# Kernel tuning notes

Measured on AMD Instinct MI355X. Metric: run time of the kernel, lower is better.

Reference implementation:

```python
import jax, jax.numpy as jnp
import numpy as np

B, T, D = 2, 2048, 2048
H, HD = 32, 64  # n_heads, head_dim; H*HD == attn_dim == D


def _rope(x, cos, sin):
    # x: (B,T,H,HD) with interleaved (real, imag) pairs on last dim
    b, t, h, hd = x.shape
    x2 = x.reshape(b, t, h, hd // 2, 2)
    xr, xi = x2[..., 0], x2[..., 1]
    c = cos[None, :, None, :]  # (1,T,1,HD/2)
    s = sin[None, :, None, :]
    out_r = xr * c - xi * s
    out_i = xr * s + xi * c
    return jnp.stack([out_r, out_i], axis=-1).reshape(b, t, h, hd)


def setup_inputs() -> dict:
    key = jax.random.key(0)
    ks = jax.random.split(key, 5)
    x = jax.random.normal(ks[0], (B, T, D), dtype=jnp.float32)
    scale = 0.02
    wq = jax.random.normal(ks[1], (D, D), dtype=jnp.float32) * scale
    wk = jax.random.normal(ks[2], (D, D), dtype=jnp.float32) * scale
    wv = jax.random.normal(ks[3], (D, D), dtype=jnp.float32) * scale
    wo = jax.random.normal(ks[4], (D, D), dtype=jnp.float32) * scale
    # standard RoPE frequencies, theta = 10000
    inv_freq = 1.0 / (10000.0 ** (jnp.arange(0, HD, 2, dtype=jnp.float32) / HD))  # (HD/2,)
    angles = jnp.arange(T, dtype=jnp.float32)[:, None] * inv_freq[None, :]  # (T, HD/2)
    return {
        "x": x,
        "freqs_cos": jnp.cos(angles),
        "freqs_sin": jnp.sin(angles),
        "wq": wq, "wk": wk, "wv": wv, "wo": wo,
    }


def reference(x, freqs_cos, freqs_sin, wq, wk, wv, wo):
    b, t, d = x.shape
    # fused-style QKV projections (nn.Linear: x @ W.T, no bias)
    q = (x @ wq.T).reshape(b, t, H, HD)
    k = (x @ wk.T).reshape(b, t, H, HD)
    v = (x @ wv.T).reshape(b, t, H, HD)
    q = _rope(q, freqs_cos, freqs_sin)
    k = _rope(k, freqs_cos, freqs_sin)
    # causal SDPA, scale = 1/sqrt(head_dim)
    scale = 1.0 / jnp.sqrt(jnp.float32(HD))
    scores = jnp.einsum("bqhd,bkhd->bhqk", q, k) * scale  # (B,H,T,T)
    causal = jnp.tril(jnp.ones((t, t), dtype=bool))
    scores = jnp.where(causal[None, None], scores, jnp.float32(-jnp.inf))
    attn = jax.nn.softmax(scores, axis=-1)
    y = jnp.einsum("bhqk,bkhd->bqhd", attn, v).reshape(b, t, H * HD)
    return y @ wo.T
```

## Files before the change

### kernel.cpp

```cpp
#include <hip/hip_runtime.h>
#include <hip/hip_bf16.h>
#include <stdint.h>


typedef __bf16 bf16_t;
typedef __bf16 bf16x4 __attribute__((ext_vector_type(4)));
typedef __bf16 bf16x8 __attribute__((ext_vector_type(8)));
typedef float  f32x4  __attribute__((ext_vector_type(4)));

constexpr int B_ = 2, T_ = 2048, D_ = 2048, H_ = 32, HD_ = 64;
constexpr int M_ = B_ * T_;

__device__ __forceinline__ void async_copy16(const bf16_t* g, bf16_t* l) {
  __builtin_amdgcn_global_load_lds(
      (const __attribute__((address_space(1))) void*)g,
      (__attribute__((address_space(3))) void*)l, 16, 0, 0);
}

__global__ __launch_bounds__(256) void cast_f32_bf16(
    const float* __restrict__ src, bf16_t* __restrict__ dst, int n4)
{
  const int i = blockIdx.x * 256 + threadIdx.x;
  if (i >= n4) return;
  const float4 v = ((const float4*)src)[i];
  bf16x4 o;
  o[0] = (bf16_t)v.x; o[1] = (bf16_t)v.y; o[2] = (bf16_t)v.z; o[3] = (bf16_t)v.w;
  ((bf16x4*)dst)[i] = o;
}

template <typename OutT>
__global__ __launch_bounds__(256, 2) void gemm_bt(
    const bf16_t* __restrict__ A, const bf16_t* __restrict__ B,
    OutT* __restrict__ C, int M, int N, int K)
{
  __shared__ __attribute__((aligned(16))) bf16_t As[128 * 32];
  __shared__ __attribute__((aligned(16))) bf16_t Bs[128 * 32];

  const int tid    = threadIdx.x;
  const int w      = tid >> 6;
  const int l      = tid & 63;
  const int quad   = l >> 4;
  const int lane16 = l & 15;
  const int bm0 = blockIdx.x * 128;
  const int bn0 = blockIdx.y * 128;
  const int wm  = (w >> 1) * 64;
  const int wn  = (w & 1) * 64;
  const int srow = l >> 2;
  const int scol = (l & 3) * 8;

  const bf16_t* Ag = A + (size_t)bm0 * K;
  const bf16_t* Bg = B + (size_t)bn0 * K;

  f32x4 acc[4][4] = {};

  for (int kk = 0; kk < K; kk += 32) {
    __syncthreads();
#pragma unroll
    for (int s0 = 0; s0 < 2; ++s0) {
      const int s = w + s0 * 4;
      async_copy16(Ag + (size_t)(s * 16 + srow) * K + kk + scol, &As[s * 512]);
      async_copy16(Bg + (size_t)(s * 16 + srow) * K + kk + scol, &Bs[s * 512]);
    }
    __syncthreads();

    bf16x8 af[4], bfr[4];
#pragma unroll
    for (int i = 0; i < 4; ++i)
      af[i] = *(const bf16x8*)&As[(wm + i * 16 + lane16) * 32 + quad * 8];
#pragma unroll
    for (int j = 0; j < 4; ++j)
      bfr[j] = *(const bf16x8*)&Bs[(wn + j * 16 + lane16) * 32 + quad * 8];
#pragma unroll
    for (int i = 0; i < 4; ++i)
#pragma unroll
      for (int j = 0; j < 4; ++j)
        acc[i][j] = __builtin_amdgcn_mfma_f32_16x16x32_bf16(af[i], bfr[j],
                                                            acc[i][j], 0, 0, 0);
  }

#pragma unroll
  for (int i = 0; i < 4; ++i) {
#pragma unroll
    for (int r = 0; r < 4; ++r) {
      const size_t row = (size_t)(bm0 + wm + i * 16 + quad * 4 + r);
#pragma unroll
      for (int j = 0; j < 4; ++j) {
        const int col = bn0 + wn + j * 16 + lane16;
        C[row * N + col] = (OutT)acc[i][j][r];
      }
    }
  }
}

__global__ __launch_bounds__(256) void rope_kernel(
    bf16_t* __restrict__ q, bf16_t* __restrict__ k,
    const float* __restrict__ cosb, const float* __restrict__ sinb, int npair)
{
  const int idx = blockIdx.x * 256 + threadIdx.x;
  if (idx >= npair) return;
  const int p = idx & 31;
  const int t = (idx >> 10) & (T_ - 1);
  const float c = cosb[t * 32 + p];
  const float s = sinb[t * 32 + p];
  const size_t off = (size_t)idx * 2;

  const float qr = (float)q[off], qi = (float)q[off + 1];
  q[off]     = (bf16_t)((qr * c - qi * s) * 0.125f);
  q[off + 1] = (bf16_t)((qr * s + qi * c) * 0.125f);

  const float kr = (float)k[off], ki = (float)k[off + 1];
  k[off]     = (bf16_t)(kr * c - ki * s);
  k[off + 1] = (bf16_t)(kr * s + ki * c);
}

__global__ __launch_bounds__(256, 3) void flash_attn(
    const bf16_t* __restrict__ Q, const bf16_t* __restrict__ K,
    const bf16_t* __restrict__ V, bf16_t* __restrict__ Y)
{
  __shared__ __attribute__((aligned(16))) bf16_t Kf[4096];
  __shared__ __attribute__((aligned(16))) bf16_t Vf[4096];
  __shared__ __attribute__((aligned(16))) bf16_t Pt[4 * 2 * 16 * 68];

  const int tid    = threadIdx.x;
  const int w      = tid >> 6;
  const int l      = tid & 63;
  const int quad   = l >> 4;
  const int lane16 = l & 15;
  const int bh = blockIdx.y;
  const int b  = bh >> 5;
  const int h  = bh & 31;
  const int q0 = ((int)gridDim.x - 1 - (int)blockIdx.x) * 128;
  const int qa = q0 + w * 32;
  const size_t rs = (size_t)H_ * HD_;

  const bf16_t* Qb = Q + ((size_t)b * T_) * rs + h * HD_;
  const bf16_t* Kb = K + ((size_t)b * T_) * rs + h * HD_;
  const bf16_t* Vb = V + ((size_t)b * T_) * rs + h * HD_;

  bf16x8 qf[2][2];
#pragma unroll
  for (int t = 0; t < 2; ++t)
#pragma unroll
    for (int c = 0; c < 2; ++c)
      qf[t][c] = *(const bf16x8*)(Qb + (size_t)(qa + t * 16 + lane16) * rs +
                                  c * 32 + quad * 8);

  f32x4 o[2][4] = {};
  float lsum[2] = {0.f, 0.f};

  const int koff = tid >> 3;
  const int oct  = tid & 7;
  const int d0   = oct * 8;
  const int kc = oct >> 2, kq = oct & 3;
  const int nV = oct >> 1, base16 = (oct & 1) * 8;

  bf16_t* const PtW = Pt + w * (2 * 16 * 68);

  const int nsteps = q0 / 64 + 2;

  bf16x8 kr[2], vr[2];
#pragma unroll
  for (int hf = 0; hf < 2; ++hf) {
    const int key = hf * 32 + koff;
    kr[hf] = *(const bf16x8*)(Kb + (size_t)key * rs + d0);
    vr[hf] = *(const bf16x8*)(Vb + (size_t)key * rs + d0);
  }

  for (int it = 0; it < nsteps; ++it) {
    const int k0 = it * 64;
    __syncthreads();
#pragma unroll
    for (int hf = 0; hf < 2; ++hf) {
      const int key = hf * 32 + koff;
      const int gK = ((kc * 4 + (key >> 4)) * 16 + (key & 15)) * 4 + kq;
      *(bf16x8*)&Kf[gK * 8] = kr[hf];
      const int cV = key >> 5, qV = (key >> 3) & 3, jV = key & 7;
#pragma unroll
      for (int i = 0; i < 8; ++i) {
        const int g = ((cV * 4 + nV) * 16 + base16 + i) * 4 + qV;
        Vf[(g ^ oct) * 8 + jV] = vr[hf][i];
      }
    }
    __syncthreads();
    if (it + 1 < nsteps) {
      const int k0n = k0 + 64;
#pragma unroll
      for (int hf = 0; hf < 2; ++hf) {
        const int key = k0n + hf * 32 + koff;
        kr[hf] = *(const bf16x8*)(Kb + (size_t)key * rs + d0);
        vr[hf] = *(const bf16x8*)(Vb + (size_t)key * rs + d0);
      }
    }

    if (k0 > qa + 31) continue;

    f32x4 stx[4][2] = {};
#pragma unroll
    for (int c = 0; c < 2; ++c) {
#pragma unroll
      for (int kt = 0; kt < 4; ++kt) {
        const bf16x8 kfr =
            *(const bf16x8*)&Kf[(((c * 4 + kt) * 16 + lane16) * 4 + quad) * 8];
        stx[kt][0] = __builtin_amdgcn_mfma_f32_16x16x32_bf16(kfr, qf[0][c],
                                                             stx[kt][0], 0, 0, 0);
        stx[kt][1] = __builtin_amdgcn_mfma_f32_16x16x32_bf16(kfr, qf[1][c],
                                                             stx[kt][1], 0, 0, 0);
      }
    }

#pragma unroll
    for (int t = 0; t < 2; ++t) {
      const int qbase = qa + t * 16;
#pragma unroll
      for (int kt = 0; kt < 4; ++kt) {
        const int kbase = k0 + kt * 16 + quad * 4;
        const bool anymask = (k0 + kt * 16 + 15) > qbase;
        float p[4];
#pragma unroll
        for (int r = 0; r < 4; ++r) {
          float s = stx[kt][t][r];
          if (anymask) s = (kbase + r > qbase + lane16) ? -1e30f : s;
          p[r] = __expf(s);
        }
        lsum[t] += (p[0] + p[1]) + (p[2] + p[3]);
        bf16x4 pv;
        pv[0] = (bf16_t)p[0]; pv[1] = (bf16_t)p[1];
        pv[2] = (bf16_t)p[2]; pv[3] = (bf16_t)p[3];
        *(bf16x4*)&PtW[(t * 16 + lane16) * 68 + kt * 16 + quad * 4] = pv;
      }
    }

#pragma unroll
    for (int c = 0; c < 2; ++c) {
      const bf16x8 pf0 = *(const bf16x8*)&PtW[(0 * 16 + lane16) * 68 + c * 32 + quad * 8];
      const bf16x8 pf1 = *(const bf16x8*)&PtW[(1 * 16 + lane16) * 68 + c * 32 + quad * 8];
#pragma unroll
      for (int n = 0; n < 4; ++n) {
        const int g = ((c * 4 + n) * 16 + lane16) * 4 + quad;
        const int swz = n * 2 + (lane16 >> 3);
        const bf16x8 vfr = *(const bf16x8*)&Vf[(g ^ swz) * 8];
        o[0][n] = __builtin_amdgcn_mfma_f32_16x16x32_bf16(pf0, vfr, o[0][n], 0, 0, 0);
        o[1][n] = __builtin_amdgcn_mfma_f32_16x16x32_bf16(pf1, vfr, o[1][n], 0, 0, 0);
      }
    }
  }

  bf16_t* Yb = Y + ((size_t)b * T_) * rs + h * HD_;
#pragma unroll
  for (int t = 0; t < 2; ++t) {
    float lt = lsum[t];
    lt += __shfl_xor(lt, 16);
    lt += __shfl_xor(lt, 32);
#pragma unroll
    for (int r = 0; r < 4; ++r) {
      const float linv = 1.0f / __shfl(lt, quad * 4 + r);
      const size_t row = (size_t)(qa + t * 16 + quad * 4 + r);
#pragma unroll
      for (int n = 0; n < 4; ++n)
        Yb[row * rs + n * 16 + lane16] = (bf16_t)(o[t][n][r] * linv);
    }
  }
}

extern "C" void kernel_launch(void* const* d_in, const int* in_sizes, int n_in,
                              void* d_out, int out_size, void* d_ws, size_t ws_size,
                              hipStream_t stream)
{
  (void)in_sizes; (void)n_in; (void)out_size; (void)ws_size;
  const float* x  = (const float*)d_in[0];
  const float* fc = (const float*)d_in[1];
  const float* fs = (const float*)d_in[2];
  const float* wq = (const float*)d_in[3];
  const float* wk = (const float*)d_in[4];
  const float* wv = (const float*)d_in[5];
  const float* wo = (const float*)d_in[6];
  float* out = (float*)d_out;

  const size_t nx = (size_t)M_ * D_;
  const size_t nw = (size_t)D_ * D_;
  bf16_t* ws = (bf16_t*)d_ws;
  bf16_t* wb = ws;
  bf16_t* xb = ws + nw;
  bf16_t* qb = xb + nx;
  bf16_t* kb = qb + nx;
  bf16_t* vb = kb + nx;
  bf16_t* yb = xb;

  const dim3 blk(256);
  const dim3 gg(M_ / 128, D_ / 128);
  const int nx4 = (int)(nx / 4), nw4 = (int)(nw / 4);

  cast_f32_bf16<<<dim3(nx4 / 256), blk, 0, stream>>>(x, xb, nx4);

  cast_f32_bf16<<<dim3(nw4 / 256), blk, 0, stream>>>(wq, wb, nw4);
  gemm_bt<bf16_t><<<gg, blk, 0, stream>>>(xb, wb, qb, M_, D_, D_);
  cast_f32_bf16<<<dim3(nw4 / 256), blk, 0, stream>>>(wk, wb, nw4);
  gemm_bt<bf16_t><<<gg, blk, 0, stream>>>(xb, wb, kb, M_, D_, D_);
  cast_f32_bf16<<<dim3(nw4 / 256), blk, 0, stream>>>(wv, wb, nw4);
  gemm_bt<bf16_t><<<gg, blk, 0, stream>>>(xb, wb, vb, M_, D_, D_);

  rope_kernel<<<dim3((B_ * T_ * H_ * 32) / 256), blk, 0, stream>>>(
      qb, kb, fc, fs, B_ * T_ * H_ * 32);
  flash_attn<<<dim3(T_ / 128, B_ * H_), blk, 0, stream>>>(qb, kb, vb, yb);

  cast_f32_bf16<<<dim3(nw4 / 256), blk, 0, stream>>>(wo, wb, nw4);
  gemm_bt<float><<<gg, blk, 0, stream>>>(yb, wb, out, M_, D_, D_);
}
```

Before: 502.5 us.

## Fuse QKV projections into one GEMM and pair causal query tiles in attention

The three separate Q/K/V projection GEMMs become one launch over a concatenated bf16 weight buffer (48 column tiles), with each tile routed to the Q, K or V output. This removes two launches and the wave-quantization tail of three small grids, at the cost of a larger workspace, with a fallback path when the workspace is too small. Flash attention now has each block handle two query tiles (gx and 15-gx), so every block does a similar amount of causal work and each K/V tile loaded to LDS is reused for both. Occupancy drops to 2 blocks per CU because of the doubled register state.

```diff
diff --git a/kernel.cpp b/kernel.cpp
--- a/kernel.cpp
+++ b/kernel.cpp
@@ -92,6 +92,70 @@
   }
 }
 
+__global__ __launch_bounds__(256, 2) void gemm_qkv(
+    const bf16_t* __restrict__ A, const bf16_t* __restrict__ B,
+    bf16_t* __restrict__ Cq, bf16_t* __restrict__ Ck, bf16_t* __restrict__ Cv,
+    int M, int K)
+{
+  __shared__ __attribute__((aligned(16))) bf16_t As[128 * 32];
+  __shared__ __attribute__((aligned(16))) bf16_t Bs[128 * 32];
+
+  const int tid    = threadIdx.x;
+  const int w      = tid >> 6;
+  const int l      = tid & 63;
+  const int quad   = l >> 4;
+  const int lane16 = l & 15;
+  const int bm0 = blockIdx.x * 128;
+  const int bn0 = blockIdx.y * 128;
+  const int wm  = (w >> 1) * 64;
+  const int wn  = (w & 1) * 64;
+  const int srow = l >> 2;
+  const int scol = (l & 3) * 8;
+
+  const bf16_t* Ag = A + (size_t)bm0 * K;
+  const bf16_t* Bg = B + (size_t)bn0 * K;
+
+  f32x4 acc[4][4] = {};
+
+  for (int kk = 0; kk < K; kk += 32) {
+    __syncthreads();
+#pragma unroll
+    for (int s0 = 0; s0 < 2; ++s0) {
+      const int s = w + s0 * 4;
+      async_copy16(Ag + (size_t)(s * 16 + srow) * K + kk + scol, &As[s * 512]);
+      async_copy16(Bg + (size_t)(s * 16 + srow) * K + kk + scol, &Bs[s * 512]);
+    }
+    __syncthreads();
+
+    bf16x8 af[4], bfr[4];
+#pragma unroll
+    for (int i = 0; i < 4; ++i)
+      af[i] = *(const bf16x8*)&As[(wm + i * 16 + lane16) * 32 + quad * 8];
+#pragma unroll
+    for (int j = 0; j < 4; ++j)
+      bfr[j] = *(const bf16x8*)&Bs[(wn + j * 16 + lane16) * 32 + quad * 8];
+#pragma unroll
+    for (int i = 0; i < 4; ++i)
+#pragma unroll
+      for (int j = 0; j < 4; ++j)
+        acc[i][j] = __builtin_amdgcn_mfma_f32_16x16x32_bf16(af[i], bfr[j],
+                                                            acc[i][j], 0, 0, 0);
+  }
+
+  bf16_t* Cb = (bn0 < 2048) ? Cq : (bn0 < 4096) ? Ck : Cv;
+  const int cb0 = (bn0 & 2047) + wn;
+#pragma unroll
+  for (int i = 0; i < 4; ++i) {
+#pragma unroll
+    for (int r = 0; r < 4; ++r) {
+      const size_t row = (size_t)(bm0 + wm + i * 16 + quad * 4 + r);
+#pragma unroll
+      for (int j = 0; j < 4; ++j)
+        Cb[row * 2048 + cb0 + j * 16 + lane16] = (bf16_t)acc[i][j][r];
+    }
+  }
+}
+
 __global__ __launch_bounds__(256) void rope_kernel(
     bf16_t* __restrict__ q, bf16_t* __restrict__ k,
     const float* __restrict__ cosb, const float* __restrict__ sinb, int npair)
@@ -113,7 +177,7 @@
   k[off + 1] = (bf16_t)(kr * s + ki * c);
 }
 
-__global__ __launch_bounds__(256, 3) void flash_attn(
+__global__ __launch_bounds__(256, 2) void flash_attn(
     const bf16_t* __restrict__ Q, const bf16_t* __restrict__ K,
     const bf16_t* __restrict__ V, bf16_t* __restrict__ Y)
 {
@@ -129,24 +193,28 @@
   const int bh = blockIdx.y;
   const int b  = bh >> 5;
   const int h  = bh & 31;
-  const int q0 = ((int)gridDim.x - 1 - (int)blockIdx.x) * 128;
-  const int qa = q0 + w * 32;
+  const int gx = blockIdx.x;
+  int qa[2];
+  qa[0] = gx * 128 + w * 32;
+  qa[1] = (15 - gx) * 128 + w * 32;
   const size_t rs = (size_t)H_ * HD_;
 
   const bf16_t* Qb = Q + ((size_t)b * T_) * rs + h * HD_;
   const bf16_t* Kb = K + ((size_t)b * T_) * rs + h * HD_;
   const bf16_t* Vb = V + ((size_t)b * T_) * rs + h * HD_;
 
-  bf16x8 qf[2][2];
-#pragma unroll
-  for (int t = 0; t < 2; ++t)
-#pragma unroll
-    for (int c = 0; c < 2; ++c)
-      qf[t][c] = *(const bf16x8*)(Qb + (size_t)(qa + t * 16 + lane16) * rs +
-                                  c * 32 + quad * 8);
-
-  f32x4 o[2][4] = {};
-  float lsum[2] = {0.f, 0.f};
+  bf16x8 qf[2][2][2];
+#pragma unroll
+  for (int g = 0; g < 2; ++g)
+#pragma unroll
+    for (int t = 0; t < 2; ++t)
+#pragma unroll
+      for (int c = 0; c < 2; ++c)
+        qf[g][t][c] = *(const bf16x8*)(Qb + (size_t)(qa[g] + t * 16 + lane16) * rs +
+                                       c * 32 + quad * 8);
+
+  f32x4 o[2][2][4] = {};
+  float lsum[2][2] = {};
 
   const int koff = tid >> 3;
   const int oct  = tid & 7;
@@ -156,7 +224,7 @@
 
   bf16_t* const PtW = Pt + w * (2 * 16 * 68);
 
-  const int nsteps = q0 / 64 + 2;
+  const int nsteps = (15 - gx) * 2 + 2;
 
   bf16x8 kr[2], vr[2];
 #pragma unroll
@@ -177,8 +245,8 @@
       const int cV = key >> 5, qV = (key >> 3) & 3, jV = key & 7;
 #pragma unroll
       for (int i = 0; i < 8; ++i) {
-        const int g = ((cV * 4 + nV) * 16 + base16 + i) * 4 + qV;
-        Vf[(g ^ oct) * 8 + jV] = vr[hf][i];
+        const int gv = ((cV * 4 + nV) * 16 + base16 + i) * 4 + qV;
+        Vf[(gv ^ oct) * 8 + jV] = vr[hf][i];
       }
     }
     __syncthreads();
@@ -192,72 +260,78 @@
       }
     }
 
-    if (k0 > qa + 31) continue;
-
-    f32x4 stx[4][2] = {};
-#pragma unroll
-    for (int c = 0; c < 2; ++c) {
-#pragma unroll
-      for (int kt = 0; kt < 4; ++kt) {
-        const bf16x8 kfr =
-            *(const bf16x8*)&Kf[(((c * 4 + kt) * 16 + lane16) * 4 + quad) * 8];
-        stx[kt][0] = __builtin_amdgcn_mfma_f32_16x16x32_bf16(kfr, qf[0][c],
-                                                             stx[kt][0], 0, 0, 0);
-        stx[kt][1] = __builtin_amdgcn_mfma_f32_16x16x32_bf16(kfr, qf[1][c],
-                                                             stx[kt][1], 0, 0, 0);
-      }
-    }
-
+#pragma unroll
+    for (int g = 0; g < 2; ++g) {
+      if (k0 > qa[g] + 31) continue;
+
+      f32x4 stx[4][2] = {};
+#pragma unroll
+      for (int c = 0; c < 2; ++c) {
+#pragma unroll
+        for (int kt = 0; kt < 4; ++kt) {
+          const bf16x8 kfr =
+              *(const bf16x8*)&Kf[(((c * 4 + kt) * 16 + lane16) * 4 + quad) * 8];
+          stx[kt][0] = __builtin_amdgcn_mfma_f32_16x16x32_bf16(kfr, qf[g][0][c],
+                                                               stx[kt][0], 0, 0, 0);
+          stx[kt][1] = __builtin_amdgcn_mfma_f32_16x16x32_bf16(kfr, qf[g][1][c],
+                                                               stx[kt][1], 0, 0, 0);
+        }
+      }
+
+#pragma unroll
+      for (int t = 0; t < 2; ++t) {
+        const int qbase = qa[g] + t * 16;
+#pragma unroll
+        for (int kt = 0; kt < 4; ++kt) {
+          const int kbase = k0 + kt * 16 + quad * 4;
+          const bool anymask = (k0 + kt * 16 + 15) > qbase;
+          float p[4];
+#pragma unroll
+          for (int r = 0; r < 4; ++r) {
+            float s = stx[kt][t][r];
+            if (anymask) s = (kbase + r > qbase + lane16) ? -1e30f : s;
+            p[r] = __expf(s);
+          }
+          lsum[g][t] += (p[0] + p[1]) + (p[2] + p[3]);
+          bf16x4 pv;
+          pv[0] = (bf16_t)p[0]; pv[1] = (bf16_t)p[1];
+          pv[2] = (bf16_t)p[2]; pv[3] = (bf16_t)p[3];
+          *(bf16x4*)&PtW[(t * 16 + lane16) * 68 + kt * 16 + quad * 4] = pv;
+        }
+      }
+
+#pragma unroll
+      for (int c = 0; c < 2; ++c) {
+        const bf16x8 pf0 = *(const bf16x8*)&PtW[(0 * 16 + lane16) * 68 + c * 32 + quad * 8];
+        const bf16x8 pf1 = *(const bf16x8*)&PtW[(1 * 16 + lane16) * 68 + c * 32 + quad * 8];
+#pragma unroll
+        for (int n = 0; n < 4; ++n) {
+          const int gv = ((c * 4 + n) * 16 + lane16) * 4 + quad;
+          const int swz = n * 2 + (lane16 >> 3);
+          const bf16x8 vfr = *(const bf16x8*)&Vf[(gv ^ swz) * 8];
+          o[g][0][n] = __builtin_amdgcn_mfma_f32_16x16x32_bf16(pf0, vfr, o[g][0][n], 0, 0, 0);
+          o[g][1][n] = __builtin_amdgcn_mfma_f32_16x16x32_bf16(pf1, vfr, o[g][1][n], 0, 0, 0);
+        }
+      }
+    }
+  }
+
+  bf16_t* Yb = Y + ((size_t)b * T_) * rs + h * HD_;
+#pragma unroll
+  for (int g = 0; g < 2; ++g) {
 #pragma unroll
     for (int t = 0; t < 2; ++t) {
-      const int qbase = qa + t * 16;
-#pragma unroll
-      for (int kt = 0; kt < 4; ++kt) {
-        const int kbase = k0 + kt * 16 + quad * 4;
-        const bool anymask = (k0 + kt * 16 + 15) > qbase;
-        float p[4];
-#pragma unroll
-        for (int r = 0; r < 4; ++r) {
-          float s = stx[kt][t][r];
-          if (anymask) s = (kbase + r > qbase + lane16) ? -1e30f : s;
-          p[r] = __expf(s);
-        }
-        lsum[t] += (p[0] + p[1]) + (p[2] + p[3]);
-        bf16x4 pv;
-        pv[0] = (bf16_t)p[0]; pv[1] = (bf16_t)p[1];
-        pv[2] = (bf16_t)p[2]; pv[3] = (bf16_t)p[3];
-        *(bf16x4*)&PtW[(t * 16 + lane16) * 68 + kt * 16 + quad * 4] = pv;
-      }
-    }
-
-#pragma unroll
-    for (int c = 0; c < 2; ++c) {
-      const bf16x8 pf0 = *(const bf16x8*)&PtW[(0 * 16 + lane16) * 68 + c * 32 + quad * 8];
-      const bf16x8 pf1 = *(const bf16x8*)&PtW[(1 * 16 + lane16) * 68 + c * 32 + quad * 8];
-#pragma unroll
-      for (int n = 0; n < 4; ++n) {
-        const int g = ((c * 4 + n) * 16 + lane16) * 4 + quad;
-        const int swz = n * 2 + (lane16 >> 3);
-        const bf16x8 vfr = *(const bf16x8*)&Vf[(g ^ swz) * 8];
-        o[0][n] = __builtin_amdgcn_mfma_f32_16x16x32_bf16(pf0, vfr, o[0][n], 0, 0, 0);
-        o[1][n] = __builtin_amdgcn_mfma_f32_16x16x32_bf16(pf1, vfr, o[1][n], 0, 0, 0);
-      }
-    }
-  }
-
-  bf16_t* Yb = Y + ((size_t)b * T_) * rs + h * HD_;
-#pragma unroll
-  for (int t = 0; t < 2; ++t) {
-    float lt = lsum[t];
-    lt += __shfl_xor(lt, 16);
-    lt += __shfl_xor(lt, 32);
-#pragma unroll
-    for (int r = 0; r < 4; ++r) {
-      const float linv = 1.0f / __shfl(lt, quad * 4 + r);
-      const size_t row = (size_t)(qa + t * 16 + quad * 4 + r);
-#pragma unroll
-      for (int n = 0; n < 4; ++n)
-        Yb[row * rs + n * 16 + lane16] = (bf16_t)(o[t][n][r] * linv);
+      float lt = lsum[g][t];
+      lt += __shfl_xor(lt, 16);
+      lt += __shfl_xor(lt, 32);
+#pragma unroll
+      for (int r = 0; r < 4; ++r) {
+        const float linv = 1.0f / __shfl(lt, quad * 4 + r);
+        const size_t row = (size_t)(qa[g] + t * 16 + quad * 4 + r);
+#pragma unroll
+        for (int n = 0; n < 4; ++n)
+          Yb[row * rs + n * 16 + lane16] = (bf16_t)(o[g][t][n][r] * linv);
+      }
     }
   }
 }
@@ -266,7 +340,7 @@
                               void* d_out, int out_size, void* d_ws, size_t ws_size,
                               hipStream_t stream)
 {
-  (void)in_sizes; (void)n_in; (void)out_size; (void)ws_size;
+  (void)in_sizes; (void)n_in; (void)out_size;
   const float* x  = (const float*)d_in[0];
   const float* fc = (const float*)d_in[1];
   const float* fs = (const float*)d_in[2];
@@ -278,31 +352,54 @@
 
   const size_t nx = (size_t)M_ * D_;
   const size_t nw = (size_t)D_ * D_;
-  bf16_t* ws = (bf16_t*)d_ws;
-  bf16_t* wb = ws;
-  bf16_t* xb = ws + nw;
-  bf16_t* qb = xb + nx;
-  bf16_t* kb = qb + nx;
-  bf16_t* vb = kb + nx;
-  bf16_t* yb = xb;
-
   const dim3 blk(256);
+  const int nx4 = (int)(nx / 4), nw4 = (int)(nw / 4);
   const dim3 gg(M_ / 128, D_ / 128);
-  const int nx4 = (int)(nx / 4), nw4 = (int)(nw / 4);
-
-  cast_f32_bf16<<<dim3(nx4 / 256), blk, 0, stream>>>(x, xb, nx4);
-
-  cast_f32_bf16<<<dim3(nw4 / 256), blk, 0, stream>>>(wq, wb, nw4);
-  gemm_bt<bf16_t><<<gg, blk, 0, stream>>>(xb, wb, qb, M_, D_, D_);
-  cast_f32_bf16<<<dim3(nw4 / 256), blk, 0, stream>>>(wk, wb, nw4);
-  gemm_bt<bf16_t><<<gg, blk, 0, stream>>>(xb, wb, kb, M_, D_, D_);
-  cast_f32_bf16<<<dim3(nw4 / 256), blk, 0, stream>>>(wv, wb, nw4);
-  gemm_bt<bf16_t><<<gg, blk, 0, stream>>>(xb, wb, vb, M_, D_, D_);
-
-  rope_kernel<<<dim3((B_ * T_ * H_ * 32) / 256), blk, 0, stream>>>(
-      qb, kb, fc, fs, B_ * T_ * H_ * 32);
-  flash_attn<<<dim3(T_ / 128, B_ * H_), blk, 0, stream>>>(qb, kb, vb, yb);
-
-  cast_f32_bf16<<<dim3(nw4 / 256), blk, 0, stream>>>(wo, wb, nw4);
-  gemm_bt<float><<<gg, blk, 0, stream>>>(yb, wb, out, M_, D_, D_);
-}
+
+  if (ws_size >= (3 * nw + 4 * nx) * sizeof(bf16_t)) {
+    bf16_t* ws  = (bf16_t*)d_ws;
+    bf16_t* wb3 = ws;
+    bf16_t* xb  = ws + 3 * nw;
+    bf16_t* qb  = xb + nx;
+    bf16_t* kb  = qb + nx;
+    bf16_t* vb  = kb + nx;
+    bf16_t* yb  = xb;
+
+    cast_f32_bf16<<<dim3(nx4 / 256), blk, 0, stream>>>(x, xb, nx4);
+    cast_f32_bf16<<<dim3(nw4 / 256), blk, 0, stream>>>(wq, wb3, nw4);
+    cast_f32_bf16<<<dim3(nw4 / 256), blk, 0, stream>>>(wk, wb3 + nw, nw4);
+    cast_f32_bf16<<<dim3(nw4 / 256), blk, 0, stream>>>(wv, wb3 + 2 * nw, nw4);
+
+    gemm_qkv<<<dim3(M_ / 128, 48), blk, 0, stream>>>(xb, wb3, qb, kb, vb, M_, D_);
+
+    rope_kernel<<<dim3((B_ * T_ * H_ * 32) / 256), blk, 0, stream>>>(
+        qb, kb, fc, fs, B_ * T_ * H_ * 32);
+    flash_attn<<<dim3(8, B_ * H_), blk, 0, stream>>>(qb, kb, vb, yb);
+
+    cast_f32_bf16<<<dim3(nw4 / 256), blk, 0, stream>>>(wo, wb3, nw4);
+    gemm_bt<float><<<gg, blk, 0, stream>>>(yb, wb3, out, M_, D_, D_);
+  } else {
+    bf16_t* ws = (bf16_t*)d_ws;
+    bf16_t* wb = ws;
+    bf16_t* xb = ws + nw;
+    bf16_t* qb = xb + nx;
+    bf16_t* kb = qb + nx;
+    bf16_t* vb = kb + nx;
+    bf16_t* yb = xb;
+
+    cast_f32_bf16<<<dim3(nx4 / 256), blk, 0, stream>>>(x, xb, nx4);
+    cast_f32_bf16<<<dim3(nw4 / 256), blk, 0, stream>>>(wq, wb, nw4);
+    gemm_bt<bf16_t><<<gg, blk, 0, stream>>>(xb, wb, qb, M_, D_, D_);
+    cast_f32_bf16<<<dim3(nw4 / 256), blk, 0, stream>>>(wk, wb, nw4);
+    gemm_bt<bf16_t><<<gg, blk, 0, stream>>>(xb, wb, kb, M_, D_, D_);
+    cast_f32_bf16<<<dim3(nw4 / 256), blk, 0, stream>>>(wv, wb, nw4);
+    gemm_bt<bf16_t><<<gg, blk, 0, stream>>>(xb, wb, vb, M_, D_, D_);
+
+    rope_kernel<<<dim3((B_ * T_ * H_ * 32) / 256), blk, 0, stream>>>(
+        qb, kb, fc, fs, B_ * T_ * H_ * 32);
+    flash_attn<<<dim3(8, B_ * H_), blk, 0, stream>>>(qb, kb, vb, yb);
+
+    cast_f32_bf16<<<dim3(nw4 / 256), blk, 0, stream>>>(wo, wb, nw4);
+    gemm_bt<float><<<gg, blk, 0, stream>>>(yb, wb, out, M_, D_, D_);
+  }
+}
```

Result: faster. 413.4 us (-17.7%).
